# Performance work log

Hardware: AMD Instinct MI355X
Metric: run time of the kernel (lower is better)

The kernel has to match this reference:

```python
import jax, jax.numpy as jnp
import numpy as np

IN_FEATURES = 256
OUT_FEATURES = 4096
BATCH = 8192


def _build_expansion_mapping():
    # out_feature j is a copy of in_feature j // (OUT_FEATURES // IN_FEATURES)
    k = OUT_FEATURES // IN_FEATURES
    em = np.zeros((OUT_FEATURES, IN_FEATURES), dtype=np.float32)
    em[np.arange(OUT_FEATURES), np.arange(OUT_FEATURES) // k] = 1.0
    return jnp.asarray(em)


def setup_inputs() -> dict:
    key = jax.random.key(0)
    x = jax.random.normal(key, (BATCH, IN_FEATURES), dtype=jnp.float32)
    return {
        "x": x,
        "expansion_mapping": _build_expansion_mapping(),
        "means": jnp.zeros((OUT_FEATURES,), dtype=jnp.float32),
        "vars_": jnp.ones((OUT_FEATURES,), dtype=jnp.float32),
        "coefs": jnp.ones((OUT_FEATURES,), dtype=jnp.float32),
    }


def reference(x, expansion_mapping, means, vars_, coefs):
    # (E @ x^T)^T == x @ E^T : [B, F_out]
    xe = jnp.einsum('bi,oi->bo', x, expansion_mapping)
    z = (xe - means) / vars_
    return jnp.exp(-0.5 * z * z) * coefs
```

## Files before the change

### kernel.cpp

```cpp
#include <hip/hip_runtime.h>
#include <hip/hip_bf16.h>

#define IN_F 256
#define OUT_F 4096
#define BATCH 8192
#define B_PER_BLOCK 16

typedef float v4f __attribute__((ext_vector_type(4)));

__global__ __launch_bounds__(256) void urbf_build_idx(
    const float* __restrict__ em, int* __restrict__ idx) {
    const int wave = blockIdx.x * (blockDim.x >> 6) + (threadIdx.x >> 6);
    const int lane = threadIdx.x & 63;
    if (wave >= OUT_F) return;
    const float* row = em + (size_t)wave * IN_F;
    int found = 0;
    #pragma unroll
    for (int c = 0; c < IN_F; c += 64) {
        const float v = row[c + lane];
        const unsigned long long m = __ballot(v != 0.0f);
        if (m) found = c + (int)(__ffsll((unsigned long long)m) - 1);
    }
    if (lane == 0) idx[wave] = found;
}

__global__ __launch_bounds__(256) void urbf_main(
    const float* __restrict__ x, const int* __restrict__ idx,
    const float* __restrict__ means, const float* __restrict__ vars_,
    const float* __restrict__ coefs, float* __restrict__ out) {
    const int j4 = blockIdx.x * 256 + threadIdx.x;
    const int j  = j4 << 2;

    const int4   si = *(const int4*)(idx + j);
    const float4 mu = *(const float4*)(means + j);
    const float4 vv = *(const float4*)(vars_ + j);
    const float4 cc = *(const float4*)(coefs + j);

    const float C = -0.72134752044448170368f;
    float4 a;
    {
        float4 r;
        r.x = __frcp_rn(vv.x); r.y = __frcp_rn(vv.y);
        r.z = __frcp_rn(vv.z); r.w = __frcp_rn(vv.w);
        a.x = C * r.x * r.x; a.y = C * r.y * r.y;
        a.z = C * r.z * r.z; a.w = C * r.w * r.w;
    }

    const int b0 = blockIdx.y * B_PER_BLOCK;
    #pragma unroll 4
    for (int bb = 0; bb < B_PER_BLOCK; ++bb) {
        const int b = b0 + bb;
        const float* xrow = x + (size_t)b * IN_F;
        const float x0 = xrow[si.x];
        const float x1 = xrow[si.y];
        const float x2 = xrow[si.z];
        const float x3 = xrow[si.w];

        v4f o; float d;
        d = x0 - mu.x; o.x = exp2f(d * d * a.x) * cc.x;
        d = x1 - mu.y; o.y = exp2f(d * d * a.y) * cc.y;
        d = x2 - mu.z; o.z = exp2f(d * d * a.z) * cc.z;
        d = x3 - mu.w; o.w = exp2f(d * d * a.w) * cc.w;

        __builtin_nontemporal_store(o, (v4f*)(out + (size_t)b * OUT_F + j));
    }
}

extern "C" void kernel_launch(void* const* d_in, const int* in_sizes, int n_in,
                              void* d_out, int out_size, void* d_ws, size_t ws_size,
                              hipStream_t stream) {
    const float* x     = (const float*)d_in[0];
    const float* em    = (const float*)d_in[1];
    const float* means = (const float*)d_in[2];
    const float* vars_ = (const float*)d_in[3];
    const float* coefs = (const float*)d_in[4];
    float* out = (float*)d_out;
    int* idx = (int*)d_ws;

    urbf_build_idx<<<OUT_F / 4, 256, 0, stream>>>(em, idx);

    dim3 grid(OUT_F / 4 / 256, BATCH / B_PER_BLOCK);
    urbf_main<<<grid, 256, 0, stream>>>(x, idx, means, vars_, coefs, out);
}
```

Measured before the change: 164.1 us.

## Restructure main kernel to row blocks with uniform-index fast path

Each block now covers 8 full batch rows across all 4096 outputs, with every thread owning four column groups whose parameters are loaded once per block. When the four indices in a group are equal, x is loaded once per group instead of four times. The idx builder switches to one float4 load plus a single ballot and a lane shuffle. Nontemporal stores become normal stores and exp2f is swapped for the hardware exp2 builtin, which may change how the write-dominated output moves through cache.

```diff
diff --git a/kernel.cpp b/kernel.cpp
--- a/kernel.cpp
+++ b/kernel.cpp
@@ -1,10 +1,9 @@
 #include <hip/hip_runtime.h>
-#include <hip/hip_bf16.h>
 
 #define IN_F 256
 #define OUT_F 4096
 #define BATCH 8192
-#define B_PER_BLOCK 16
+#define ROWS_PER_BLOCK 8
 
 typedef float v4f __attribute__((ext_vector_type(4)));
 
@@ -13,56 +12,84 @@
     const int wave = blockIdx.x * (blockDim.x >> 6) + (threadIdx.x >> 6);
     const int lane = threadIdx.x & 63;
     if (wave >= OUT_F) return;
-    const float* row = em + (size_t)wave * IN_F;
-    int found = 0;
-    #pragma unroll
-    for (int c = 0; c < IN_F; c += 64) {
-        const float v = row[c + lane];
-        const unsigned long long m = __ballot(v != 0.0f);
-        if (m) found = c + (int)(__ffsll((unsigned long long)m) - 1);
-    }
-    if (lane == 0) idx[wave] = found;
+    const float4 v = *(const float4*)(em + (size_t)wave * IN_F + lane * 4);
+    const bool nz = (v.x != 0.0f) | (v.y != 0.0f) | (v.z != 0.0f) | (v.w != 0.0f);
+    const unsigned long long m = __ballot(nz);
+    const int sub = (v.x != 0.0f) ? 0 : (v.y != 0.0f) ? 1 : (v.z != 0.0f) ? 2 : 3;
+    const int src = m ? (int)(__ffsll(m) - 1) : 0;
+    const int subs = __shfl(sub, src);
+    if (lane == 0) idx[wave] = m ? src * 4 + subs : 0;
 }
 
 __global__ __launch_bounds__(256) void urbf_main(
     const float* __restrict__ x, const int* __restrict__ idx,
     const float* __restrict__ means, const float* __restrict__ vars_,
     const float* __restrict__ coefs, float* __restrict__ out) {
-    const int j4 = blockIdx.x * 256 + threadIdx.x;
-    const int j  = j4 << 2;
+    const int t = threadIdx.x;
+    const float C = -0.72134752044448170368f;
 
-    const int4   si = *(const int4*)(idx + j);
-    const float4 mu = *(const float4*)(means + j);
-    const float4 vv = *(const float4*)(vars_ + j);
-    const float4 cc = *(const float4*)(coefs + j);
-
-    const float C = -0.72134752044448170368f;
-    float4 a;
-    {
+    int    sis[4];
+    float4 mu[4], a[4], cc[4];
+    bool uniform = true;
+    #pragma unroll
+    for (int jj = 0; jj < 4; ++jj) {
+        const int j = jj * 1024 + t * 4;
+        const int4 si = *(const int4*)(idx + j);
+        sis[jj] = si.x;
+        uniform = uniform & (si.x == si.y) & (si.x == si.z) & (si.x == si.w);
+        mu[jj] = *(const float4*)(means + j);
+        cc[jj] = *(const float4*)(coefs + j);
+        const float4 vv = *(const float4*)(vars_ + j);
         float4 r;
         r.x = __frcp_rn(vv.x); r.y = __frcp_rn(vv.y);
         r.z = __frcp_rn(vv.z); r.w = __frcp_rn(vv.w);
-        a.x = C * r.x * r.x; a.y = C * r.y * r.y;
-        a.z = C * r.z * r.z; a.w = C * r.w * r.w;
+        a[jj].x = C * r.x * r.x; a[jj].y = C * r.y * r.y;
+        a[jj].z = C * r.z * r.z; a[jj].w = C * r.w * r.w;
     }
 
-    const int b0 = blockIdx.y * B_PER_BLOCK;
-    #pragma unroll 4
-    for (int bb = 0; bb < B_PER_BLOCK; ++bb) {
-        const int b = b0 + bb;
-        const float* xrow = x + (size_t)b * IN_F;
-        const float x0 = xrow[si.x];
-        const float x1 = xrow[si.y];
-        const float x2 = xrow[si.z];
-        const float x3 = xrow[si.w];
+    const int b0 = blockIdx.x * ROWS_PER_BLOCK;
+    const float* xb = x + (size_t)b0 * IN_F;
+    float* ob = out + (size_t)b0 * OUT_F + t * 4;
 
-        v4f o; float d;
-        d = x0 - mu.x; o.x = exp2f(d * d * a.x) * cc.x;
-        d = x1 - mu.y; o.y = exp2f(d * d * a.y) * cc.y;
-        d = x2 - mu.z; o.z = exp2f(d * d * a.z) * cc.z;
-        d = x3 - mu.w; o.w = exp2f(d * d * a.w) * cc.w;
-
-        __builtin_nontemporal_store(o, (v4f*)(out + (size_t)b * OUT_F + j));
+    if (uniform) {
+        float xs[ROWS_PER_BLOCK][4];
+        #pragma unroll
+        for (int r = 0; r < ROWS_PER_BLOCK; ++r) {
+            #pragma unroll
+            for (int jj = 0; jj < 4; ++jj)
+                xs[r][jj] = xb[r * IN_F + sis[jj]];
+        }
+        #pragma unroll
+        for (int r = 0; r < ROWS_PER_BLOCK; ++r) {
+            float* op = ob + (size_t)r * OUT_F;
+            #pragma unroll
+            for (int jj = 0; jj < 4; ++jj) {
+                const float xv = xs[r][jj];
+                v4f o; float d;
+                d = xv - mu[jj].x; o.x = __builtin_amdgcn_exp2f(d * d * a[jj].x) * cc[jj].x;
+                d = xv - mu[jj].y; o.y = __builtin_amdgcn_exp2f(d * d * a[jj].y) * cc[jj].y;
+                d = xv - mu[jj].z; o.z = __builtin_amdgcn_exp2f(d * d * a[jj].z) * cc[jj].z;
+                d = xv - mu[jj].w; o.w = __builtin_amdgcn_exp2f(d * d * a[jj].w) * cc[jj].w;
+                *(v4f*)(op + jj * 1024) = o;
+            }
+        }
+    } else {
+        #pragma unroll
+        for (int r = 0; r < ROWS_PER_BLOCK; ++r) {
+            const float* xrow = xb + (size_t)r * IN_F;
+            float* op = ob + (size_t)r * OUT_F;
+            #pragma unroll
+            for (int jj = 0; jj < 4; ++jj) {
+                const int j = jj * 1024 + t * 4;
+                const int4 si = *(const int4*)(idx + j);
+                v4f o; float d;
+                d = xrow[si.x] - mu[jj].x; o.x = __builtin_amdgcn_exp2f(d * d * a[jj].x) * cc[jj].x;
+                d = xrow[si.y] - mu[jj].y; o.y = __builtin_amdgcn_exp2f(d * d * a[jj].y) * cc[jj].y;
+                d = xrow[si.z] - mu[jj].z; o.z = __builtin_amdgcn_exp2f(d * d * a[jj].z) * cc[jj].z;
+                d = xrow[si.w] - mu[jj].w; o.w = __builtin_amdgcn_exp2f(d * d * a[jj].w) * cc[jj].w;
+                *(v4f*)(op + jj * 1024) = o;
+            }
+        }
     }
 }
 
@@ -79,6 +106,5 @@
 
     urbf_build_idx<<<OUT_F / 4, 256, 0, stream>>>(em, idx);
 
-    dim3 grid(OUT_F / 4 / 256, BATCH / B_PER_BLOCK);
-    urbf_main<<<grid, 256, 0, stream>>>(x, idx, means, vars_, coefs, out);
+    urbf_main<<<BATCH / ROWS_PER_BLOCK, 256, 0, stream>>>(x, idx, means, vars_, coefs, out);
 }
```

Result: faster. 151.5 us (median of 2 runs) (-7.7%).
